# Performance work log

Measured on AMD Instinct MI355X. Metric: run time of the kernel, lower is better.

The kernel has to match this reference:

```python
import jax, jax.numpy as jnp
import numpy as np

B, S, D, H = 4, 2048, 1024, 16
HD = D // H


def setup_inputs() -> dict:
    key = jax.random.key(0)
    ks = jax.random.split(key, 9)
    s = 0.02  # GPT-2 init scale for weights
    return {
        "hidden_states": jax.random.normal(ks[0], (B, S, D), jnp.float32),
        "Wq": jax.random.normal(ks[1], (D, D), jnp.float32) * s,
        "bq": jnp.zeros((D,), jnp.float32),
        "Wk": jax.random.normal(ks[2], (D, D), jnp.float32) * s,
        "bk": jnp.zeros((D,), jnp.float32),
        "Wv": jax.random.normal(ks[3], (D, D), jnp.float32) * s,
        "bv": jnp.zeros((D,), jnp.float32),
        "Wo": jax.random.normal(ks[4], (D, D), jnp.float32) * s,
        "bo": jnp.zeros((D,), jnp.float32),
    }


def _split_heads(x):
    b, s, _ = x.shape
    return x.reshape(b, s, H, HD).transpose(0, 2, 1, 3)  # [B,H,S,HD]


def reference(hidden_states, Wq, bq, Wk, bk, Wv, bv, Wo, bo):
    b, s, d = hidden_states.shape
    q = _split_heads(hidden_states @ Wq + bq)
    k = _split_heads(hidden_states @ Wk + bk)
    v = _split_heads(hidden_states @ Wv + bv)
    # naive attention: full [B,H,S,S] scores, scale, causal where-mask, softmax, AV
    scores = jnp.einsum('bhqd,bhkd->bhqk', q, k)
    scores = scores / jnp.asarray(HD, scores.dtype) ** 0.5  # scale_attn_weights
    causal = jnp.tril(jnp.ones((s, s), dtype=bool))  # bias buffer slice
    scores = jnp.where(causal, scores, jnp.finfo(scores.dtype).min)
    attn = jax.nn.softmax(scores, axis=-1)  # attn_dropout p=0 -> identity
    out = jnp.einsum('bhqk,bhkd->bhqd', attn, v)
    out = out.transpose(0, 2, 1, 3).reshape(b, s, d)  # merge heads
    return out @ Wo + bo  # resid_dropout p=0 -> identity
```

## Files before the change

### kernel.cpp

```cpp
#include <hip/hip_runtime.h>
#include <stdint.h>


#define GAS __attribute__((address_space(1)))
#define LAS __attribute__((address_space(3)))

typedef __attribute__((ext_vector_type(4))) float f32x4;
typedef __attribute__((ext_vector_type(8))) short bf16x8;

__device__ __forceinline__ short f2bf(float f) {
  union { float f; uint32_t u; } v; v.f = f;
  uint32_t r = v.u + 0x7fffu + ((v.u >> 16) & 1u);
  return (short)(r >> 16);
}

__device__ __forceinline__ float bf2f(short s) {
  union { uint32_t u; float f; } v;
  v.u = ((uint32_t)(uint16_t)s) << 16;
  return v.f;
}

__device__ __forceinline__ uint32_t cvt_pk_bf16(float lo, float hi) {
  uint32_t r;
  asm("v_cvt_pk_bf16_f32 %0, %1, %2" : "=v"(r) : "v"(lo), "v"(hi));
  return r;
}

__device__ __forceinline__ void gload_lds16(const void* g, void* l) {
  __builtin_amdgcn_global_load_lds((const GAS void*)g, (LAS void*)l, 16, 0, 0);
}

#define GATE(N)                                            \
  __builtin_amdgcn_sched_barrier(0);                       \
  asm volatile("s_waitcnt vmcnt(" #N ")" ::: "memory");    \
  __builtin_amdgcn_s_barrier();                            \
  __builtin_amdgcn_sched_barrier(0);

__global__ __launch_bounds__(256) void cvt_bf16_kernel(const float* __restrict__ in,
                                                       short* __restrict__ out, int n4) {
  int i = blockIdx.x * blockDim.x + threadIdx.x;
  int stride = gridDim.x * blockDim.x;
  for (int idx = i; idx < n4; idx += stride) {
    float4 v = ((const float4*)in)[idx];
    short4 o;
    o.x = f2bf(v.x); o.y = f2bf(v.y); o.z = f2bf(v.z); o.w = f2bf(v.w);
    ((short4*)out)[idx] = o;
  }
}

__global__ __launch_bounds__(256) void wt4_kernel(const float* __restrict__ W0,
                                                  const float* __restrict__ W1,
                                                  const float* __restrict__ W2,
                                                  const float* __restrict__ W3,
                                                  short* __restrict__ Wt) {
  __shared__ short tile[64][65];
  const float* W = (blockIdx.z == 0) ? W0 : (blockIdx.z == 1) ? W1
                   : (blockIdx.z == 2) ? W2 : W3;
  short* dst = Wt + ((size_t)blockIdx.z << 20);
  const int k0 = blockIdx.x * 64, n0 = blockIdx.y * 64;
  const int t = threadIdx.x;
#pragma unroll
  for (int i = 0; i < 16; ++i) {
    int r = (t >> 6) + i * 4, c = t & 63;
    tile[r][c] = f2bf(W[(size_t)(k0 + r) * 1024 + n0 + c]);
  }
  __syncthreads();
#pragma unroll
  for (int i = 0; i < 16; ++i) {
    int r = (t >> 6) + i * 4, c = t & 63;
    dst[(size_t)(n0 + r) * 1024 + k0 + c] = tile[c][r];
  }
}

template <int MODE>
__global__ __launch_bounds__(512, 2) void gemm2(const short* __restrict__ A,
                                                const short* __restrict__ Bt,
                                                const float* __restrict__ b0,
                                                const float* __restrict__ b1,
                                                const float* __restrict__ b2,
                                                void* __restrict__ O0,
                                                void* __restrict__ O1,
                                                void* __restrict__ O2) {
  __shared__ short lds[4][12288];
  const int xcd = (int)blockIdx.x & 7;
  const int t = (int)blockIdx.x >> 3;
  const int m0 = (xcd * 4 + (t & 3)) * 256;
  const int n0 = (t >> 2) * 128;
  const int tid = threadIdx.x;
  const int lane = tid & 63, w = tid >> 6;
  const int l15 = lane & 15, lg = lane >> 4;
  const int wm = w >> 1, wn = w & 1;

  const short* ag[2];
  const short* bg;
#pragma unroll
  for (int i = 0; i < 2; ++i) {
    const int P = w * 64 + i * 512 + lane;
    const int L = P ^ ((P >> 3) & 7);
    ag[i] = A + (size_t)(m0 + (L >> 2)) * 1024 + (L & 3) * 8;
  }
  {
    const int P = w * 64 + lane;
    const int L = P ^ ((P >> 3) & 7);
    bg = Bt + (size_t)(n0 + (L >> 2)) * 1024 + (L & 3) * 8;
  }

  int aof[4], bof[4];
#pragma unroll
  for (int mf = 0; mf < 4; ++mf) {
    const int L = (wm * 64 + mf * 16 + l15) * 4 + lg;
    aof[mf] = (L ^ ((L >> 3) & 7)) * 8;
  }
#pragma unroll
  for (int nf = 0; nf < 4; ++nf) {
    const int L = (wn * 64 + nf * 16 + l15) * 4 + lg;
    bof[nf] = (L ^ ((L >> 3) & 7)) * 8;
  }

  f32x4 acc[4][4];
#pragma unroll
  for (int i = 0; i < 4; ++i)
#pragma unroll
    for (int j = 0; j < 4; ++j) acc[i][j] = (f32x4){0.f, 0.f, 0.f, 0.f};

  auto stage = [&](int bi, int kt) {
    short* As = &lds[bi][0];
    short* Bs = &lds[bi][8192];
#pragma unroll
    for (int i = 0; i < 2; ++i)
      gload_lds16(ag[i] + kt * 32, As + (w * 64 + i * 512) * 8);
    gload_lds16(bg + kt * 32, Bs + (w * 64) * 8);
  };

  auto compute = [&](int bi) {
    const short* As = &lds[bi][0];
    const short* Bs = &lds[bi][8192];
    bf16x8 a[4], b[4];
#pragma unroll
    for (int mf = 0; mf < 4; ++mf) a[mf] = *(const bf16x8*)&As[aof[mf]];
#pragma unroll
    for (int nf = 0; nf < 4; ++nf) b[nf] = *(const bf16x8*)&Bs[bof[nf]];
    __builtin_amdgcn_s_setprio(1);
#pragma unroll
    for (int mf = 0; mf < 4; ++mf)
#pragma unroll
      for (int nf = 0; nf < 4; ++nf)
        acc[mf][nf] =
            __builtin_amdgcn_mfma_f32_16x16x32_bf16(a[mf], b[nf], acc[mf][nf], 0, 0, 0);
    __builtin_amdgcn_s_setprio(0);
  };

  stage(0, 0);
  stage(1, 1);
  stage(2, 2);

  for (int j = 0; j < 29; ++j) {
    GATE(6)
    stage((j + 3) & 3, j + 3);
    compute(j & 3);
  }
  GATE(6) compute(1);
  GATE(3) compute(2);
  GATE(0) compute(3);

  if (MODE == 1) {
    float* dst = (float*)O0;
#pragma unroll
    for (int mf = 0; mf < 4; ++mf)
#pragma unroll
      for (int nf = 0; nf < 4; ++nf) {
        const int col = n0 + wn * 64 + nf * 16 + l15;
        const float bv = b0[col];
#pragma unroll
        for (int rr = 0; rr < 4; ++rr) {
          const int row = m0 + wm * 64 + mf * 16 + lg * 4 + rr;
          dst[(size_t)row * 1024 + col] = acc[mf][nf][rr] + bv;
        }
      }
  } else {
    const int mat = n0 >> 10;
    const int nc0 = n0 & 1023;
    const float* bias = (mat == 0) ? b0 : (mat == 1) ? b1 : b2;
    if (mat < 2) {
      short* dst = (short*)(mat == 0 ? O0 : O1);
#pragma unroll
      for (int mf = 0; mf < 4; ++mf)
#pragma unroll
        for (int nf = 0; nf < 4; ++nf) {
          const int col = nc0 + wn * 64 + nf * 16 + l15;
          const float bv = bias[col];
          const int h = col >> 6, hd = col & 63;
#pragma unroll
          for (int rr = 0; rr < 4; ++rr) {
            const int row = m0 + wm * 64 + mf * 16 + lg * 4 + rr;
            const int b = row >> 11, s = row & 2047;
            dst[((size_t)(b * 16 + h) * 2048 + s) * 64 + hd] = f2bf(acc[mf][nf][rr] + bv);
          }
        }
    } else {
      short* dst = (short*)O2;
#pragma unroll
      for (int mf = 0; mf < 4; ++mf) {
        const int rowb = m0 + wm * 64 + mf * 16 + lg * 4;
        const int b = rowb >> 11, s = rowb & 2047;
        const int s2 = (s & ~31) | (((s >> 2) & 3) << 3) | (((s >> 4) & 1) << 2);
#pragma unroll
        for (int nf = 0; nf < 4; ++nf) {
          const int col = nc0 + wn * 64 + nf * 16 + l15;
          const float bv = bias[col];
          const int h = col >> 6, hd = col & 63;
          short4 sv;
          sv.x = f2bf(acc[mf][nf][0] + bv);
          sv.y = f2bf(acc[mf][nf][1] + bv);
          sv.z = f2bf(acc[mf][nf][2] + bv);
          sv.w = f2bf(acc[mf][nf][3] + bv);
          *(short4*)&dst[((size_t)(b * 16 + h) * 64 + hd) * 2048 + s2] = sv;
        }
      }
    }
  }
}

__global__ __launch_bounds__(256) void attn_kernel(const short* __restrict__ Q,
                                                   const short* __restrict__ K,
                                                   const short* __restrict__ Vt,
                                                   short* __restrict__ Oout) {
  __shared__ short Ks[3][4096];
  __shared__ short Vs[3][4096];
  const int g = (int)blockIdx.x;
  const int bh = (((g >> 3) & 7) << 3) | (g & 7);
  const int jq = 15 - (g >> 6);
  const int q0 = jq * 128;
  const int tid = threadIdx.x;
  const int lane = tid & 63, w = tid >> 6;
  const int l15 = lane & 15, lg = lane >> 4;
  const short* Qb = Q + (size_t)bh * 2048 * 64;
  const short* Kb = K + (size_t)bh * 2048 * 64;
  const short* Vb = Vt + (size_t)bh * 64 * 2048;
  const int b = bh >> 4, h = bh & 15;
  const float SC = 0.18033688011112042f;
  const int qg0 = q0 + w * 32;

  bf16x8 qf[2][2];
#pragma unroll
  for (int qs = 0; qs < 2; ++qs)
#pragma unroll
    for (int kk = 0; kk < 2; ++kk) {
      bf16x8 rq =
          *(const bf16x8*)&Qb[(size_t)(qg0 + qs * 16 + l15) * 64 + kk * 32 + lg * 8];
      union { uint32_t u[4]; bf16x8 v; } sq;
#pragma unroll
      for (int d = 0; d < 4; ++d)
        sq.u[d] = cvt_pk_bf16(bf2f(rq[2 * d]) * SC, bf2f(rq[2 * d + 1]) * SC);
      qf[qs][kk] = sq.v;
    }

  union { short s[8]; bf16x8 v; } one_u;
#pragma unroll
  for (int i = 0; i < 8; ++i) one_u.s[i] = (short)0x3F80;

  const short* kg[2];
  const short* vg[2];
#pragma unroll
  for (int i = 0; i < 2; ++i) {
    const int P = (w * 2 + i) * 64 + lane;
    const int L = P ^ ((P >> 3) & 7);
    kg[i] = Kb + (size_t)(L >> 3) * 64 + (L & 7) * 8;
    vg[i] = Vb + (size_t)(L >> 3) * 2048 + (L & 7) * 8;
  }

  int kcol[2], vcol[2];
#pragma unroll
  for (int kk = 0; kk < 2; ++kk) {
    kcol[kk] = (((kk * 4 + lg) ^ (l15 & 7)) << 3);
    vcol[kk] = kcol[kk];
  }

  f32x4 o[2][4];
#pragma unroll
  for (int i = 0; i < 2; ++i)
#pragma unroll
    for (int j = 0; j < 4; ++j) o[i][j] = (f32x4){0.f, 0.f, 0.f, 0.f};
  f32x4 psacc[2] = {(f32x4){0.f, 0.f, 0.f, 0.f}, (f32x4){0.f, 0.f, 0.f, 0.f}};

  auto stageKV = [&](int bi, int kt) {
#pragma unroll
    for (int i = 0; i < 2; ++i) {
      gload_lds16(kg[i] + (size_t)kt * 4096, &Ks[bi][(w * 2 + i) * 512]);
      gload_lds16(vg[i] + kt * 64, &Vs[bi][(w * 2 + i) * 512]);
    }
  };

  const int nkt = 2 * jq + 2;
  stageKV(0, 0);
  stageKV(1, 1);

  int cur = 0;
  for (int kt = 0; kt < nkt; ++kt) {
    if (kt + 1 < nkt) {
      GATE(4)
    } else {
      GATE(0)
    }
    if (kt + 2 < nkt) {
      int nb = cur + 2; if (nb >= 3) nb -= 3;
      stageKV(nb, kt + 2);
    }

    if (kt * 64 <= qg0 + 31) {
      const short* Kc = &Ks[cur][0];
      const short* Vc = &Vs[cur][0];

      f32x4 sacc[4][2];
#pragma unroll
      for (int t = 0; t < 4; ++t)
#pragma unroll
        for (int qs = 0; qs < 2; ++qs) sacc[t][qs] = (f32x4){0.f, 0.f, 0.f, 0.f};
      __builtin_amdgcn_s_setprio(1);
#pragma unroll
      for (int t = 0; t < 4; ++t) {
        const int krow = (t * 16 + l15) * 64;
#pragma unroll
        for (int kk = 0; kk < 2; ++kk) {
          bf16x8 kf = *(const bf16x8*)&Kc[krow + kcol[kk]];
#pragma unroll
          for (int qs = 0; qs < 2; ++qs)
            sacc[t][qs] = __builtin_amdgcn_mfma_f32_16x16x32_bf16(kf, qf[qs][kk],
                                                                  sacc[t][qs], 0, 0, 0);
        }
      }
      __builtin_amdgcn_s_setprio(0);

      if (kt * 64 + 63 > qg0) {
#pragma unroll
        for (int t = 0; t < 4; ++t)
#pragma unroll
          for (int qs = 0; qs < 2; ++qs)
#pragma unroll
            for (int r = 0; r < 4; ++r) {
              const int kg_ = kt * 64 + t * 16 + lg * 4 + r;
              const int qg = qg0 + qs * 16 + l15;
              if (kg_ > qg) sacc[t][qs][r] = -3e38f;
            }
      }

      bf16x8 pa[2][2];
#pragma unroll
      for (int qs = 0; qs < 2; ++qs) {
#pragma unroll
        for (int t = 0; t < 4; ++t)
#pragma unroll
          for (int r = 0; r < 4; ++r)
            sacc[t][qs][r] = __builtin_amdgcn_exp2f(sacc[t][qs][r]);
#pragma unroll
        for (int kk = 0; kk < 2; ++kk) {
          union { uint32_t u[4]; bf16x8 v; } pw;
          pw.u[0] = cvt_pk_bf16(sacc[2 * kk][qs][0], sacc[2 * kk][qs][1]);
          pw.u[1] = cvt_pk_bf16(sacc[2 * kk][qs][2], sacc[2 * kk][qs][3]);
          pw.u[2] = cvt_pk_bf16(sacc[2 * kk + 1][qs][0], sacc[2 * kk + 1][qs][1]);
          pw.u[3] = cvt_pk_bf16(sacc[2 * kk + 1][qs][2], sacc[2 * kk + 1][qs][3]);
          pa[qs][kk] = pw.v;
        }
      }

      __builtin_amdgcn_s_setprio(1);
#pragma unroll
      for (int ds = 0; ds < 4; ++ds) {
        const int vrow = (ds * 16 + l15) * 64;
#pragma unroll
        for (int kk = 0; kk < 2; ++kk) {
          bf16x8 vf = *(const bf16x8*)&Vc[vrow + vcol[kk]];
#pragma unroll
          for (int qs = 0; qs < 2; ++qs)
            o[qs][ds] = __builtin_amdgcn_mfma_f32_16x16x32_bf16(pa[qs][kk], vf,
                                                                o[qs][ds], 0, 0, 0);
        }
      }
#pragma unroll
      for (int qs = 0; qs < 2; ++qs)
#pragma unroll
        for (int kk = 0; kk < 2; ++kk)
          psacc[qs] = __builtin_amdgcn_mfma_f32_16x16x32_bf16(pa[qs][kk], one_u.v,
                                                              psacc[qs], 0, 0, 0);
      __builtin_amdgcn_s_setprio(0);
    }

    cur = cur + 1 == 3 ? 0 : cur + 1;
  }

#pragma unroll
  for (int qs = 0; qs < 2; ++qs) {
    float inv[4];
#pragma unroll
    for (int r = 0; r < 4; ++r) inv[r] = 1.f / psacc[qs][r];
#pragma unroll
    for (int ds = 0; ds < 4; ++ds)
#pragma unroll
      for (int r = 0; r < 4; ++r) {
        const int qg = q0 + w * 32 + qs * 16 + lg * 4 + r;
        const int col = h * 64 + ds * 16 + l15;
        Oout[((size_t)(b * 2048 + qg)) * 1024 + col] = f2bf(o[qs][ds][r] * inv[r]);
      }
  }
}

extern "C" void kernel_launch(void* const* d_in, const int* in_sizes, int n_in,
                              void* d_out, int out_size, void* d_ws, size_t ws_size,
                              hipStream_t stream) {
  const float* hs = (const float*)d_in[0];
  const float* Wq = (const float*)d_in[1];
  const float* bq = (const float*)d_in[2];
  const float* Wk = (const float*)d_in[3];
  const float* bk = (const float*)d_in[4];
  const float* Wv = (const float*)d_in[5];
  const float* bv = (const float*)d_in[6];
  const float* Wo = (const float*)d_in[7];
  const float* bo = (const float*)d_in[8];

  char* ws = (char*)d_ws;
  short* Xbf = (short*)(ws + 0);
  short* Qb  = (short*)(ws + ((size_t)16 << 20));
  short* Kb  = (short*)(ws + ((size_t)32 << 20));
  short* Vtb = (short*)(ws + ((size_t)48 << 20));
  short* Wts = (short*)(ws + ((size_t)64 << 20));
  short* Wot = Wts + ((size_t)3 << 20);

  cvt_bf16_kernel<<<2048, 256, 0, stream>>>(hs, Xbf, (8192 * 1024) / 4);
  wt4_kernel<<<dim3(16, 16, 4), 256, 0, stream>>>(Wq, Wk, Wv, Wo, Wts);

  gemm2<0><<<768, 512, 0, stream>>>(Xbf, Wts, bq, bk, bv, Qb, Kb, Vtb);

  attn_kernel<<<1024, 256, 0, stream>>>(Qb, Kb, Vtb, Xbf);

  gemm2<1><<<256, 512, 0, stream>>>(Xbf, Wot, bo, nullptr, nullptr,
                                    (float*)d_out, nullptr, nullptr);
}
```

Before: 152.0 us.

## Enlarge GEMM block tile to 256x256 with split-phase ping-pong scheduling

Replaces the 256x128 GEMM tile with a 256x256 tile where each wave computes 128x64, halving the grid for both the QKV and output projections. The K loop is restructured into two MFMA phases per step, interleaving async global-to-LDS loads of the next A and B slices with barriers and priority raises. This aims to raise arithmetic intensity and LDS reuse per loaded byte. In exchange it doubles LDS per block (likely limiting residency), increases accumulator registers, and leaves fewer blocks than CUs for the output GEMM.

```diff
diff --git a/kernel.cpp b/kernel.cpp
--- a/kernel.cpp
+++ b/kernel.cpp
@@ -35,6 +35,15 @@
   asm volatile("s_waitcnt vmcnt(" #N ")" ::: "memory");    \
   __builtin_amdgcn_s_barrier();                            \
   __builtin_amdgcn_sched_barrier(0);
+
+#define PH_SYNC                                            \
+  __builtin_amdgcn_s_barrier();                            \
+  asm volatile("s_waitcnt lgkmcnt(0)" ::: "memory");       \
+  __builtin_amdgcn_sched_barrier(0);                       \
+  __builtin_amdgcn_s_setprio(1);
+#define PH_END                                             \
+  __builtin_amdgcn_s_setprio(0);                           \
+  __builtin_amdgcn_s_barrier();
 
 __global__ __launch_bounds__(256) void cvt_bf16_kernel(const float* __restrict__ in,
                                                        short* __restrict__ out, int n4) {
@@ -73,107 +82,103 @@
 }
 
 template <int MODE>
-__global__ __launch_bounds__(512, 2) void gemm2(const short* __restrict__ A,
-                                                const short* __restrict__ Bt,
-                                                const float* __restrict__ b0,
-                                                const float* __restrict__ b1,
-                                                const float* __restrict__ b2,
-                                                void* __restrict__ O0,
-                                                void* __restrict__ O1,
-                                                void* __restrict__ O2) {
-  __shared__ short lds[4][12288];
+__global__ __launch_bounds__(512, 2) void gemm256(const short* __restrict__ A,
+                                                  const short* __restrict__ Bt,
+                                                  const float* __restrict__ b0,
+                                                  const float* __restrict__ b1,
+                                                  const float* __restrict__ b2,
+                                                  void* __restrict__ O0,
+                                                  void* __restrict__ O1,
+                                                  void* __restrict__ O2) {
+  __shared__ short lds[4][16384];
   const int xcd = (int)blockIdx.x & 7;
   const int t = (int)blockIdx.x >> 3;
   const int m0 = (xcd * 4 + (t & 3)) * 256;
-  const int n0 = (t >> 2) * 128;
+  const int n0 = (t >> 2) * 256;
   const int tid = threadIdx.x;
   const int lane = tid & 63, w = tid >> 6;
   const int l15 = lane & 15, lg = lane >> 4;
-  const int wm = w >> 1, wn = w & 1;
-
-  const short* ag[2];
-  const short* bg;
-#pragma unroll
-  for (int i = 0; i < 2; ++i) {
-    const int P = w * 64 + i * 512 + lane;
-    const int L = P ^ ((P >> 3) & 7);
-    ag[i] = A + (size_t)(m0 + (L >> 2)) * 1024 + (L & 3) * 8;
-  }
+  const int wm = w >> 2, wn = w & 3;
+
+  const short* agp[2];
+  const short* bgp[2];
   {
-    const int P = w * 64 + lane;
-    const int L = P ^ ((P >> 3) & 7);
-    bg = Bt + (size_t)(n0 + (L >> 2)) * 1024 + (L & 3) * 8;
-  }
-
-  int aof[4], bof[4];
-#pragma unroll
-  for (int mf = 0; mf < 4; ++mf) {
-    const int L = (wm * 64 + mf * 16 + l15) * 4 + lg;
-    aof[mf] = (L ^ ((L >> 3) & 7)) * 8;
-  }
-#pragma unroll
-  for (int nf = 0; nf < 4; ++nf) {
-    const int L = (wn * 64 + nf * 16 + l15) * 4 + lg;
-    bof[nf] = (L ^ ((L >> 3) & 7)) * 8;
-  }
-
-  f32x4 acc[4][4];
-#pragma unroll
-  for (int i = 0; i < 4; ++i)
+    const int cl = (tid & 3) ^ ((tid >> 3) & 3);
+#pragma unroll
+    for (int i = 0; i < 2; ++i) {
+      const int r = i * 128 + (tid >> 2);
+      agp[i] = A + (size_t)(m0 + r) * 1024 + cl * 8;
+      bgp[i] = Bt + (size_t)(n0 + r) * 1024 + cl * 8;
+    }
+  }
+
+  const int ach = (lg ^ ((l15 >> 1) & 3)) * 8;
+  const int aofs = (wm * 128 + l15) * 32 + ach;
+  const int bofs = 8192 + (wn * 64 + l15) * 32 + ach;
+
+  f32x4 acc[8][4];
+#pragma unroll
+  for (int i = 0; i < 8; ++i)
 #pragma unroll
     for (int j = 0; j < 4; ++j) acc[i][j] = (f32x4){0.f, 0.f, 0.f, 0.f};
 
-  auto stage = [&](int bi, int kt) {
-    short* As = &lds[bi][0];
-    short* Bs = &lds[bi][8192];
-#pragma unroll
-    for (int i = 0; i < 2; ++i)
-      gload_lds16(ag[i] + kt * 32, As + (w * 64 + i * 512) * 8);
-    gload_lds16(bg + kt * 32, Bs + (w * 64) * 8);
+  auto stageA = [&](int s, int h, int i) {
+    gload_lds16(agp[i] + h * 32, &lds[s][i * 4096 + w * 512]);
   };
-
-  auto compute = [&](int bi) {
-    const short* As = &lds[bi][0];
-    const short* Bs = &lds[bi][8192];
-    bf16x8 a[4], b[4];
-#pragma unroll
-    for (int mf = 0; mf < 4; ++mf) a[mf] = *(const bf16x8*)&As[aof[mf]];
-#pragma unroll
-    for (int nf = 0; nf < 4; ++nf) b[nf] = *(const bf16x8*)&Bs[bof[nf]];
-    __builtin_amdgcn_s_setprio(1);
+  auto stageB = [&](int s, int h, int i) {
+    gload_lds16(bgp[i] + h * 32, &lds[s][8192 + i * 4096 + w * 512]);
+  };
+
+  stageA(0, 0, 0); stageA(0, 0, 1); stageB(0, 0, 0); stageB(0, 0, 1);
+  stageA(1, 1, 0); stageA(1, 1, 1); stageB(1, 1, 0); stageB(1, 1, 1);
+
+  for (int h = 0; h < 32; ++h) {
+    if (h < 31) { GATE(4) } else { GATE(0) }
+    const int s = h & 3;
+    const int s2 = (h + 2) & 3;
+    const bool st = (h < 30);
+    const short* sl = &lds[s][0];
+
+    bf16x8 a[4], bfr[4];
+#pragma unroll
+    for (int mf = 0; mf < 4; ++mf) a[mf] = *(const bf16x8*)&sl[aofs + mf * 512];
+#pragma unroll
+    for (int nf = 0; nf < 4; ++nf) bfr[nf] = *(const bf16x8*)&sl[bofs + nf * 512];
+    if (st) { stageA(s2, h + 2, 0); stageA(s2, h + 2, 1); }
+    PH_SYNC
 #pragma unroll
     for (int mf = 0; mf < 4; ++mf)
 #pragma unroll
       for (int nf = 0; nf < 4; ++nf)
         acc[mf][nf] =
-            __builtin_amdgcn_mfma_f32_16x16x32_bf16(a[mf], b[nf], acc[mf][nf], 0, 0, 0);
-    __builtin_amdgcn_s_setprio(0);
-  };
-
-  stage(0, 0);
-  stage(1, 1);
-  stage(2, 2);
-
-  for (int j = 0; j < 29; ++j) {
-    GATE(6)
-    stage((j + 3) & 3, j + 3);
-    compute(j & 3);
-  }
-  GATE(6) compute(1);
-  GATE(3) compute(2);
-  GATE(0) compute(3);
+            __builtin_amdgcn_mfma_f32_16x16x32_bf16(a[mf], bfr[nf], acc[mf][nf], 0, 0, 0);
+    PH_END
+
+#pragma unroll
+    for (int mf = 0; mf < 4; ++mf)
+      a[mf] = *(const bf16x8*)&sl[aofs + (mf + 4) * 512];
+    if (st) { stageB(s2, h + 2, 0); stageB(s2, h + 2, 1); }
+    PH_SYNC
+#pragma unroll
+    for (int mf = 0; mf < 4; ++mf)
+#pragma unroll
+      for (int nf = 0; nf < 4; ++nf)
+        acc[mf + 4][nf] =
+            __builtin_amdgcn_mfma_f32_16x16x32_bf16(a[mf], bfr[nf], acc[mf + 4][nf], 0, 0, 0);
+    PH_END
+  }
 
   if (MODE == 1) {
     float* dst = (float*)O0;
 #pragma unroll
-    for (int mf = 0; mf < 4; ++mf)
+    for (int mf = 0; mf < 8; ++mf)
 #pragma unroll
       for (int nf = 0; nf < 4; ++nf) {
         const int col = n0 + wn * 64 + nf * 16 + l15;
         const float bv = b0[col];
 #pragma unroll
         for (int rr = 0; rr < 4; ++rr) {
-          const int row = m0 + wm * 64 + mf * 16 + lg * 4 + rr;
+          const int row = m0 + wm * 128 + mf * 16 + lg * 4 + rr;
           dst[(size_t)row * 1024 + col] = acc[mf][nf][rr] + bv;
         }
       }
@@ -184,7 +189,7 @@
     if (mat < 2) {
       short* dst = (short*)(mat == 0 ? O0 : O1);
 #pragma unroll
-      for (int mf = 0; mf < 4; ++mf)
+      for (int mf = 0; mf < 8; ++mf)
 #pragma unroll
         for (int nf = 0; nf < 4; ++nf) {
           const int col = nc0 + wn * 64 + nf * 16 + l15;
@@ -192,7 +197,7 @@
           const int h = col >> 6, hd = col & 63;
 #pragma unroll
           for (int rr = 0; rr < 4; ++rr) {
-            const int row = m0 + wm * 64 + mf * 16 + lg * 4 + rr;
+            const int row = m0 + wm * 128 + mf * 16 + lg * 4 + rr;
             const int b = row >> 11, s = row & 2047;
             dst[((size_t)(b * 16 + h) * 2048 + s) * 64 + hd] = f2bf(acc[mf][nf][rr] + bv);
           }
@@ -200,8 +205,8 @@
     } else {
       short* dst = (short*)O2;
 #pragma unroll
-      for (int mf = 0; mf < 4; ++mf) {
-        const int rowb = m0 + wm * 64 + mf * 16 + lg * 4;
+      for (int mf = 0; mf < 8; ++mf) {
+        const int rowb = m0 + wm * 128 + mf * 16 + lg * 4;
         const int b = rowb >> 11, s = rowb & 2047;
         const int s2 = (s & ~31) | (((s >> 2) & 3) << 3) | (((s >> 4) & 1) << 2);
 #pragma unroll
@@ -428,10 +433,10 @@
   cvt_bf16_kernel<<<2048, 256, 0, stream>>>(hs, Xbf, (8192 * 1024) / 4);
   wt4_kernel<<<dim3(16, 16, 4), 256, 0, stream>>>(Wq, Wk, Wv, Wo, Wts);
 
-  gemm2<0><<<768, 512, 0, stream>>>(Xbf, Wts, bq, bk, bv, Qb, Kb, Vtb);
+  gemm256<0><<<384, 512, 0, stream>>>(Xbf, Wts, bq, bk, bv, Qb, Kb, Vtb);
 
   attn_kernel<<<1024, 256, 0, stream>>>(Qb, Kb, Vtb, Xbf);
 
-  gemm2<1><<<256, 512, 0, stream>>>(Xbf, Wot, bo, nullptr, nullptr,
-                                    (float*)d_out, nullptr, nullptr);
-}
+  gemm256<1><<<128, 512, 0, stream>>>(Xbf, Wot, bo, nullptr, nullptr,
+                                      (float*)d_out, nullptr, nullptr);
+}
```

Result: slower. 164.7 us (+8.4%).
